# Kernel optimization log

Measured on AMD Instinct MI355X. Metric: run time of the kernel, lower is better.

Reference implementation:

```python
import jax, jax.numpy as jnp
import numpy as np

N = 50000
IN_DIM = 512
HIDDEN = 64
OUT_DIM = 47
E1 = 800000
E2 = 1200000


def setup_inputs() -> dict:
    key = jax.random.key(0)
    ks = jax.random.split(key, 10)
    x = jax.random.normal(ks[0], (N, IN_DIM), dtype=jnp.float32)
    src1 = jax.random.randint(ks[1], (E1,), 0, N, dtype=jnp.int32)
    dst1 = jax.random.randint(ks[2], (E1,), 0, N, dtype=jnp.int32)
    w1 = jax.random.uniform(ks[3], (E1,), dtype=jnp.float32)
    src2 = jax.random.randint(ks[4], (E2,), 0, N, dtype=jnp.int32)
    dst2 = jax.random.randint(ks[5], (E2,), 0, N, dtype=jnp.int32)
    w2 = jax.random.uniform(ks[6], (E2,), dtype=jnp.float32)
    embed_w = jax.random.normal(ks[7], (IN_DIM, HIDDEN), dtype=jnp.float32) / np.sqrt(IN_DIM)
    embed_b = jnp.zeros((HIDDEN,), dtype=jnp.float32)
    total_dim = (2 ** 3 - 1) * HIDDEN  # k=2 -> 7*hidden
    cls_w = jax.random.normal(ks[8], (total_dim, OUT_DIM), dtype=jnp.float32) / np.sqrt(total_dim)
    cls_b = jnp.zeros((OUT_DIM,), dtype=jnp.float32)
    return {"x": x, "src1": src1, "dst1": dst1, "w1": w1,
            "src2": src2, "dst2": dst2, "w2": w2,
            "embed_w": embed_w, "embed_b": embed_b,
            "cls_w": cls_w, "cls_b": cls_b}


def _spmm(src, dst, w, h, n):
    # out[i] = sum_{e: dst[e]==i} w[e] * h[src[e]]  == sparse_adj @ h
    return jax.ops.segment_sum(w[:, None] * h[src], dst, num_segments=n)


def reference(x, src1, dst1, w1, src2, dst2, w2, embed_w, embed_b, cls_w, cls_b):
    k = 2
    # dropout is identity in eval mode
    h = jax.nn.relu(x @ embed_w + embed_b)  # [N, hidden]
    reps = [h]
    for _ in range(k):
        h1 = _spmm(src1, dst1, w1, h, N)  # strict 1-hop
        h2 = _spmm(src2, dst2, w2, h, N)  # strict 2-hop
        h = jax.nn.relu(jnp.concatenate([h1, h2], axis=1))
        reps.append(h)
    h_final = jnp.concatenate(reps, axis=1)  # [N, 7*hidden]
    return h_final @ cls_w + cls_b
```

## Files before the change

kernel.cpp:

```cpp
#include <hip/hip_runtime.h>

#define N_NODES 50000
#define IN_DIM 512
#define HIDDEN 64
#define OUT_DIM 47
#define HSTRIDE 448

#define NBINS 391
#define CAP1 3072
#define CAP2 4096
#define CHUNK 4096

typedef unsigned short u16;
typedef short v8s __attribute__((ext_vector_type(8)));
typedef float v4f __attribute__((ext_vector_type(4)));

union F4 { float4 v; float f[4]; };
union U4 { uint4 v; unsigned u[4]; };

static __device__ __forceinline__ u16 f2bf(float f) {
  unsigned u = __float_as_uint(f);
  u += 0x7fffu + ((u >> 16) & 1u);
  return (u16)(u >> 16);
}
static __device__ __forceinline__ float bf2f(u16 h) {
  return __uint_as_float(((unsigned)h) << 16);
}

__global__ __launch_bounds__(256) void conv_w(
    const float* __restrict__ embed_w, u16* __restrict__ weTh,
    u16* __restrict__ weTl, const float* __restrict__ cls_w,
    u16* __restrict__ wcTh, u16* __restrict__ wcTl) {
  int b = blockIdx.x;
  if (b < 16) {
    int tid = b * 256 + threadIdx.x;
    int col = tid >> 6;
    int k8 = (tid & 63) * 8;
#pragma unroll
    for (int j = 0; j < 8; j++) {
      float v = embed_w[(size_t)(k8 + j) * HIDDEN + col];
      u16 h = f2bf(v);
      weTh[(size_t)col * IN_DIM + k8 + j] = h;
      weTl[(size_t)col * IN_DIM + k8 + j] = f2bf(v - bf2f(h));
    }
  } else {
    int tid = (b - 16) * 256 + threadIdx.x;
    if (tid < 48 * 56) {
      int col = tid / 56;
      int k8 = (tid % 56) * 8;
#pragma unroll
      for (int j = 0; j < 8; j++) {
        float v = (col < OUT_DIM) ? cls_w[(size_t)(k8 + j) * OUT_DIM + col] : 0.f;
        u16 h = f2bf(v);
        wcTh[(size_t)col * HSTRIDE + k8 + j] = h;
        wcTl[(size_t)col * HSTRIDE + k8 + j] = f2bf(v - bf2f(h));
      }
    }
  }
}

__global__ __launch_bounds__(256) void embed_bin(
    const float* __restrict__ x, const u16* __restrict__ wTh,
    const u16* __restrict__ wTl, const float* __restrict__ bias,
    u16* __restrict__ hcat,
    const int* __restrict__ src1, const int* __restrict__ dst1,
    const float* __restrict__ w1, int E1, int c1,
    const int* __restrict__ src2, const int* __restrict__ dst2,
    const float* __restrict__ w2, int E2,
    int* __restrict__ binCursor, int2* __restrict__ stg1,
    int2* __restrict__ stg2) {
  int b = blockIdx.x;
  if (b < 782) {
    int wave = threadIdx.x >> 6, lane = threadIdx.x & 63;
    int row0 = b * 64 + wave * 16;
    int m = lane & 15, kq = lane >> 4;
    int rowA = row0 + m;
    if (rowA >= N_NODES) rowA = N_NODES - 1;
    const float* xr = x + (size_t)rowA * IN_DIM;

    v4f acc[4];
#pragma unroll
    for (int nf = 0; nf < 4; nf++) acc[nf] = (v4f){0.f, 0.f, 0.f, 0.f};

#pragma unroll 4
    for (int k0 = 0; k0 < IN_DIM; k0 += 32) {
      int kk = k0 + kq * 8;
      F4 p, qv;
      p.v = *(const float4*)(xr + kk);
      qv.v = *(const float4*)(xr + kk + 4);
      v8s a;
#pragma unroll
      for (int j = 0; j < 4; j++) {
        a[j] = (short)f2bf(p.f[j]);
        a[4 + j] = (short)f2bf(qv.f[j]);
      }
#pragma unroll
      for (int nf = 0; nf < 4; nf++) {
        int col = nf * 16 + m;
        v8s bh = *(const v8s*)(wTh + (size_t)col * IN_DIM + kk);
        v8s bl = *(const v8s*)(wTl + (size_t)col * IN_DIM + kk);
        acc[nf] = __builtin_amdgcn_mfma_f32_16x16x32_bf16(a, bh, acc[nf], 0, 0, 0);
        acc[nf] = __builtin_amdgcn_mfma_f32_16x16x32_bf16(a, bl, acc[nf], 0, 0, 0);
      }
    }

#pragma unroll
    for (int nf = 0; nf < 4; nf++) {
      int col = nf * 16 + m;
      float bv = bias[col];
#pragma unroll
      for (int reg = 0; reg < 4; reg++) {
        int rowC = row0 + kq * 4 + reg;
        if (rowC < N_NODES) {
          float v = acc[nf][reg] + bv;
          hcat[(size_t)rowC * HSTRIDE + col] = f2bf(v > 0.f ? v : 0.f);
        }
      }
    }
    return;
  }

  int q = b - 782;
  const int *src, *dst;
  const float* w;
  int E, cap;
  int2* stg;
  int* bc;
  if (q < c1) {
    src = src1; dst = dst1; w = w1; E = E1; stg = stg1; bc = binCursor; cap = CAP1;
  } else {
    q -= c1;
    src = src2; dst = dst2; w = w2; E = E2; stg = stg2; bc = binCursor + NBINS; cap = CAP2;
  }
  int e0 = q * CHUNK;
  int n = E - e0;
  if (n > CHUNK) n = CHUNK;

  __shared__ int hist[NBINS], segrel[NBINS], cur[NBINS];
  for (int i = threadIdx.x; i < NBINS; i += 256) { hist[i] = 0; cur[i] = 0; }
  __syncthreads();
  for (int t = threadIdx.x; t < n; t += 256)
    atomicAdd(&hist[dst[e0 + t] >> 7], 1);
  __syncthreads();
  for (int i = threadIdx.x; i < NBINS; i += 256) {
    int h = hist[i];
    segrel[i] = h ? atomicAdd(&bc[i], h) : 0;
  }
  __syncthreads();
  for (int t = threadIdx.x; t < n; t += 256) {
    int d = dst[e0 + t];
    int bin = d >> 7;
    int rel = segrel[bin] + atomicAdd(&cur[bin], 1);
    if (rel < cap)
      stg[(size_t)bin * cap + rel] =
          make_int2(src[e0 + t] | ((d & 127) << 16), __float_as_int(w[e0 + t]));
  }
}

__global__ __launch_bounds__(512) void binscan(const int* __restrict__ cnt,
                                               int* __restrict__ scanout) {
  const int* in = cnt + blockIdx.x * NBINS;
  int* out = scanout + blockIdx.x * NBINS;
  int tid = threadIdx.x, lane = tid & 63, wid = tid >> 6;
  __shared__ int wsum[8];
  int v0 = (tid < NBINS) ? in[tid] : 0;
  int v = v0;
#pragma unroll
  for (int off = 1; off < 64; off <<= 1) {
    int t = __shfl_up(v, off, 64);
    if (lane >= off) v += t;
  }
  if (lane == 63) wsum[wid] = v;
  __syncthreads();
  if (tid < 8) {
    int s = wsum[tid], sc = s;
#pragma unroll
    for (int off = 1; off < 8; off <<= 1) {
      int t = __shfl_up(sc, off, 8);
      if (tid >= off) sc += t;
    }
    wsum[tid] = sc - s;
  }
  __syncthreads();
  if (tid < NBINS) out[tid] = v - v0 + wsum[wid];
}

__global__ __launch_bounds__(256) void place(
    const int* __restrict__ binCursor, const int* __restrict__ binScan,
    const int2* __restrict__ stg1, int2* __restrict__ ew1,
    int* __restrict__ ep1, const int2* __restrict__ stg2,
    int2* __restrict__ ew2, int* __restrict__ ep2) {
  int pb = blockIdx.x;
  int lb = pb < NBINS ? pb : pb - NBINS;
  const int2* stg;
  int2* ew;
  int* ep;
  int cap;
  if (pb < NBINS) { stg = stg1; ew = ew1; ep = ep1; cap = CAP1; }
  else            { stg = stg2; ew = ew2; ep = ep2; cap = CAP2; }
  int cnt = binCursor[pb];
  if (cnt > cap) cnt = cap;
  int base = binScan[pb];
  const int2* seg = stg + (size_t)lb * cap;
  int node0 = lb << 7;
  int nnodes = N_NODES - node0;
  if (nnodes > 128) nnodes = 128;

  __shared__ int ncnt[128], noff[128], ncur[128];
  __shared__ int t0;
  if (threadIdx.x < 128) { ncnt[threadIdx.x] = 0; ncur[threadIdx.x] = 0; }
  __syncthreads();
  for (int t = threadIdx.x; t < cnt; t += 256)
    atomicAdd(&ncnt[(seg[t].x >> 16) & 127], 1);
  __syncthreads();
  int v0 = 0, v = 0;
  if (threadIdx.x < 128) {
    v0 = ncnt[threadIdx.x];
    v = v0;
    int lane = threadIdx.x & 63;
#pragma unroll
    for (int off = 1; off < 64; off <<= 1) {
      int t = __shfl_up(v, off, 64);
      if (lane >= off) v += t;
    }
    if (threadIdx.x == 63) t0 = v;
  }
  __syncthreads();
  if (threadIdx.x < 128) {
    int excl = v - v0 + (threadIdx.x >= 64 ? t0 : 0);
    noff[threadIdx.x] = excl;
    if (threadIdx.x < nnodes) ep[node0 + threadIdx.x] = base + excl + v0;
  }
  __syncthreads();
  for (int t = threadIdx.x; t < cnt; t += 256) {
    int2 pk = seg[t];
    int nl = (pk.x >> 16) & 127;
    int pos = base + noff[nl] + atomicAdd(&ncur[nl], 1);
    ew[pos] = make_int2(pk.x & 0xFFFF, pk.y);
  }
}

__device__ __forceinline__ void bf8_fma(const U4& r, float wt, float* a) {
#pragma unroll
  for (int i = 0; i < 4; i++) {
    a[2 * i]     += wt * __uint_as_float(r.u[i] << 16);
    a[2 * i + 1] += wt * __uint_as_float(r.u[i] & 0xffff0000u);
  }
}

template <int NT>
__global__ __launch_bounds__(256) void gather2(
    const int* __restrict__ ep1, const int2* __restrict__ ew1,
    const int* __restrict__ ep2, const int2* __restrict__ ew2,
    const u16* __restrict__ hin, u16* __restrict__ out1,
    u16* __restrict__ out2, int half_blocks) {
  int b = blockIdx.x;
  const int* ep;
  const int2* ew;
  u16* out;
  if (b < half_blocks) { ep = ep1; ew = ew1; out = out1; }
  else { b -= half_blocks; ep = ep2; ew = ew2; out = out2; }

  int tid = b * 256 + threadIdx.x;
  int node = tid / NT;
  if (node >= N_NODES) return;
  int col0 = (tid % NT) * 8;
  int s = node ? ep[node - 1] : 0;
  int e = ep[node];

  float a0[8], a1[8];
#pragma unroll
  for (int i = 0; i < 8; i++) { a0[i] = 0.f; a1[i] = 0.f; }

  int j = s;
  for (; j + 4 <= e; j += 4) {
    int2 p0 = ew[j], p1 = ew[j + 1], p2 = ew[j + 2], p3 = ew[j + 3];
    U4 r0, r1, r2, r3;
    r0.v = *(const uint4*)(hin + (size_t)p0.x * HSTRIDE + col0);
    r1.v = *(const uint4*)(hin + (size_t)p1.x * HSTRIDE + col0);
    r2.v = *(const uint4*)(hin + (size_t)p2.x * HSTRIDE + col0);
    r3.v = *(const uint4*)(hin + (size_t)p3.x * HSTRIDE + col0);
    bf8_fma(r0, __int_as_float(p0.y), a0);
    bf8_fma(r1, __int_as_float(p1.y), a1);
    bf8_fma(r2, __int_as_float(p2.y), a0);
    bf8_fma(r3, __int_as_float(p3.y), a1);
  }
  for (; j < e; j++) {
    int2 p = ew[j];
    U4 r;
    r.v = *(const uint4*)(hin + (size_t)p.x * HSTRIDE + col0);
    bf8_fma(r, __int_as_float(p.y), a0);
  }

  U4 o;
#pragma unroll
  for (int i = 0; i < 4; i++) {
    float lo = a0[2 * i] + a1[2 * i];
    float hi = a0[2 * i + 1] + a1[2 * i + 1];
    lo = lo > 0.f ? lo : 0.f;
    hi = hi > 0.f ? hi : 0.f;
    o.u[i] = ((unsigned)f2bf(hi) << 16) | (unsigned)f2bf(lo);
  }
  *(uint4*)(out + (size_t)node * HSTRIDE + col0) = o.v;
}

__global__ __launch_bounds__(256) void final_mfma(
    const u16* __restrict__ hcat, const u16* __restrict__ wTh,
    const u16* __restrict__ wTl, const float* __restrict__ bias,
    float* __restrict__ out) {
  int wave = threadIdx.x >> 6, lane = threadIdx.x & 63;
  int row0 = blockIdx.x * 64 + wave * 16;
  int m = lane & 15, kq = lane >> 4;
  int rowA = row0 + m;
  if (rowA >= N_NODES) rowA = N_NODES - 1;
  const u16* hr = hcat + (size_t)rowA * HSTRIDE;

  v4f acc[3];
#pragma unroll
  for (int nf = 0; nf < 3; nf++) acc[nf] = (v4f){0.f, 0.f, 0.f, 0.f};

#pragma unroll 2
  for (int k0 = 0; k0 < HSTRIDE; k0 += 32) {
    int kk = k0 + kq * 8;
    v8s a = *(const v8s*)(hr + kk);
#pragma unroll
    for (int nf = 0; nf < 3; nf++) {
      int col = nf * 16 + m;
      v8s bh = *(const v8s*)(wTh + (size_t)col * HSTRIDE + kk);
      v8s bl = *(const v8s*)(wTl + (size_t)col * HSTRIDE + kk);
      acc[nf] = __builtin_amdgcn_mfma_f32_16x16x32_bf16(a, bh, acc[nf], 0, 0, 0);
      acc[nf] = __builtin_amdgcn_mfma_f32_16x16x32_bf16(a, bl, acc[nf], 0, 0, 0);
    }
  }

#pragma unroll
  for (int nf = 0; nf < 3; nf++) {
    int col = nf * 16 + m;
    if (col < OUT_DIM) {
      float bv = bias[col];
#pragma unroll
      for (int reg = 0; reg < 4; reg++) {
        int rowC = row0 + kq * 4 + reg;
        if (rowC < N_NODES)
          out[(size_t)rowC * OUT_DIM + col] = acc[nf][reg] + bv;
      }
    }
  }
}

extern "C" void kernel_launch(void* const* d_in, const int* in_sizes, int n_in,
                              void* d_out, int out_size, void* d_ws,
                              size_t ws_size, hipStream_t stream) {
  const float* x       = (const float*)d_in[0];
  const int*   src1    = (const int*)d_in[1];
  const int*   dst1    = (const int*)d_in[2];
  const float* w1      = (const float*)d_in[3];
  const int*   src2    = (const int*)d_in[4];
  const int*   dst2    = (const int*)d_in[5];
  const float* w2      = (const float*)d_in[6];
  const float* embed_w = (const float*)d_in[7];
  const float* embed_b = (const float*)d_in[8];
  const float* cls_w   = (const float*)d_in[9];
  const float* cls_b   = (const float*)d_in[10];
  int E1 = in_sizes[1];
  int E2 = in_sizes[4];

  float* ws = (float*)d_ws;
  size_t off = 0;
  u16* hcat = (u16*)(ws + off); off += (size_t)N_NODES * HSTRIDE / 2;
  int2* ew1 = (int2*)(ws + off); off += (size_t)2 * E1;
  int2* ew2 = (int2*)(ws + off); off += (size_t)2 * E2;
  int* ep1 = (int*)(ws + off); off += N_NODES;
  int* ep2 = (int*)(ws + off); off += N_NODES;
  int2* stg1 = (int2*)(ws + off); off += (size_t)2 * NBINS * CAP1;
  int2* stg2 = (int2*)(ws + off); off += (size_t)2 * NBINS * CAP2;
  int* binCursor = (int*)(ws + off); off += 2 * NBINS;
  int* binScan = (int*)(ws + off); off += 2 * NBINS;
  u16* weTh = (u16*)(ws + off); off += 16384;
  u16* weTl = (u16*)(ws + off); off += 16384;
  u16* wcTh = (u16*)(ws + off); off += 10752;
  u16* wcTl = (u16*)(ws + off); off += 10752;

  int c1 = (E1 + CHUNK - 1) / CHUNK;
  int c2 = (E2 + CHUNK - 1) / CHUNK;

  hipMemsetAsync(binCursor, 0, 2 * NBINS * sizeof(int), stream);
  conv_w<<<27, 256, 0, stream>>>(embed_w, weTh, weTl, cls_w, wcTh, wcTl);
  embed_bin<<<782 + c1 + c2, 256, 0, stream>>>(
      x, weTh, weTl, embed_b, hcat,
      src1, dst1, w1, E1, c1, src2, dst2, w2, E2,
      binCursor, stg1, stg2);
  binscan<<<2, 512, 0, stream>>>(binCursor, binScan);
  place<<<2 * NBINS, 256, 0, stream>>>(binCursor, binScan,
                                       stg1, ew1, ep1, stg2, ew2, ep2);
  gather2<8><<<3126, 256, 0, stream>>>(ep1, ew1, ep2, ew2, hcat,
                                       hcat + 64, hcat + 128, 1563);
  gather2<16><<<6250, 256, 0, stream>>>(ep1, ew1, ep2, ew2, hcat + 64,
                                        hcat + 192, hcat + 320, 3125);
  final_mfma<<<782, 256, 0, stream>>>(hcat, wcTh, wcTl, cls_b, (float*)d_out);
}
```

Before: 260.7 us.

## Stage x tiles into LDS via async global_load_lds with double buffering

The embedding GEMM now reads x through direct global-to-LDS loads (global_load_lds) into a double-buffered, XOR-swizzled shared tile. Each wave fetches the next 32-column slice while running MFMAs on the current one, instead of issuing strided float4 global loads per lane. The goal is better coalescing and overlap of x traffic with MFMA work. The cost is a __syncthreads per k-step and 16 KB of LDS shared with the binning blocks, which may lower occupancy.

Result: faster. 253.4 us (-2.8%).

```diff
diff --git a/kernel.cpp b/kernel.cpp
--- a/kernel.cpp
+++ b/kernel.cpp
@@ -25,6 +25,15 @@
 }
 static __device__ __forceinline__ float bf2f(u16 h) {
   return __uint_as_float(((unsigned)h) << 16);
+}
+
+static __device__ __forceinline__ void load_lds16(const float* g, void* l) {
+  __builtin_amdgcn_global_load_lds(
+      reinterpret_cast<const __attribute__((address_space(1))) unsigned int*>(
+          reinterpret_cast<uintptr_t>(g)),
+      reinterpret_cast<__attribute__((address_space(3))) unsigned int*>(
+          reinterpret_cast<uintptr_t>(l)),
+      16, 0, 0);
 }
 
 __global__ __launch_bounds__(256) void conv_w(
@@ -69,31 +78,61 @@
     const float* __restrict__ w2, int E2,
     int* __restrict__ binCursor, int2* __restrict__ stg1,
     int2* __restrict__ stg2) {
+  __shared__ float4 xtile4[1024];
+  __shared__ int hist[NBINS], segrel[NBINS], cur[NBINS];
   int b = blockIdx.x;
   if (b < 782) {
+    float* xtile = (float*)xtile4;
     int wave = threadIdx.x >> 6, lane = threadIdx.x & 63;
-    int row0 = b * 64 + wave * 16;
+    int row0 = b * 64;
     int m = lane & 15, kq = lane >> 4;
-    int rowA = row0 + m;
-    if (rowA >= N_NODES) rowA = N_NODES - 1;
-    const float* xr = x + (size_t)rowA * IN_DIM;
+
+    int seg0 = wave * 2;
+    int sr0 = seg0 * 8 + (lane >> 3);
+    int sr1 = sr0 + 8;
+    int sc0 = (lane & 7) ^ (sr0 & 7);
+    int sc1 = (lane & 7) ^ (sr1 & 7);
+    int gr0 = row0 + sr0; if (gr0 >= N_NODES) gr0 = N_NODES - 1;
+    int gr1 = row0 + sr1; if (gr1 >= N_NODES) gr1 = N_NODES - 1;
+    const float* g0 = x + (size_t)gr0 * IN_DIM + sc0 * 4;
+    const float* g1 = x + (size_t)gr1 * IN_DIM + sc1 * 4;
 
     v4f acc[4];
 #pragma unroll
     for (int nf = 0; nf < 4; nf++) acc[nf] = (v4f){0.f, 0.f, 0.f, 0.f};
 
-#pragma unroll 4
-    for (int k0 = 0; k0 < IN_DIM; k0 += 32) {
-      int kk = k0 + kq * 8;
-      F4 p, qv;
-      p.v = *(const float4*)(xr + kk);
-      qv.v = *(const float4*)(xr + kk + 4);
+    int r = wave * 16 + m;
+    int slotA = (2 * kq) ^ (r & 7);
+    int slotB = slotA ^ 1;
+    const float* rbase0 = (const float*)xtile + r * 32;
+    const float* rbase1 = rbase0 + 2048;
+
+    load_lds16(g0, (char*)xtile + seg0 * 1024 + (lane & 7) * 0 + 0 + (size_t)0 +
+                       (sr0 - seg0 * 8) * 0);
+    __syncthreads();
+
+    load_lds16(g1, (char*)xtile + (seg0 + 1) * 1024);
+    __syncthreads();
+
+#pragma unroll 2
+    for (int t = 0; t < 16; t++) {
+      if (t < 15) {
+        int k0n = (t + 1) * 32;
+        int bufn = (t + 1) & 1;
+        load_lds16(g0 + k0n, (char*)xtile + bufn * 8192 + seg0 * 1024);
+        load_lds16(g1 + k0n, (char*)xtile + bufn * 8192 + (seg0 + 1) * 1024);
+      }
+      const float* rb = (t & 1) ? rbase1 : rbase0;
+      F4 p, q;
+      p.v = *(const float4*)(rb + slotA * 4);
+      q.v = *(const float4*)(rb + slotB * 4);
       v8s a;
 #pragma unroll
       for (int j = 0; j < 4; j++) {
         a[j] = (short)f2bf(p.f[j]);
-        a[4 + j] = (short)f2bf(qv.f[j]);
-      }
+        a[4 + j] = (short)f2bf(q.f[j]);
+      }
+      int kk = t * 32 + kq * 8;
 #pragma unroll
       for (int nf = 0; nf < 4; nf++) {
         int col = nf * 16 + m;
@@ -102,6 +141,7 @@
         acc[nf] = __builtin_amdgcn_mfma_f32_16x16x32_bf16(a, bh, acc[nf], 0, 0, 0);
         acc[nf] = __builtin_amdgcn_mfma_f32_16x16x32_bf16(a, bl, acc[nf], 0, 0, 0);
       }
+      __syncthreads();
     }
 
 #pragma unroll
@@ -110,7 +150,7 @@
       float bv = bias[col];
 #pragma unroll
       for (int reg = 0; reg < 4; reg++) {
-        int rowC = row0 + kq * 4 + reg;
+        int rowC = row0 + wave * 16 + kq * 4 + reg;
         if (rowC < N_NODES) {
           float v = acc[nf][reg] + bv;
           hcat[(size_t)rowC * HSTRIDE + col] = f2bf(v > 0.f ? v : 0.f);
@@ -136,7 +176,6 @@
   int n = E - e0;
   if (n > CHUNK) n = CHUNK;
 
-  __shared__ int hist[NBINS], segrel[NBINS], cur[NBINS];
   for (int i = threadIdx.x; i < NBINS; i += 256) { hist[i] = 0; cur[i] = 0; }
   __syncthreads();
   for (int t = threadIdx.x; t < n; t += 256)
```

## Split embed and binning kernels; locally sort edges in LDS before coalesced staging writes

Applied to the files above, without the earlier changes.

Splits the fused embed+binning kernel into two separate launches. Edge binning now uses a smaller chunk, holds packed edges in registers, runs a block-wide prefix scan over the bin histogram, and scatters edges into an LDS buffer sorted by bin. Staging writes then go out as contiguous per-bin runs rather than scattered stores. The cost is an extra kernel launch, twice as many binning blocks competing on the global bin-cursor atomics, and the loss of overlap between the embed GEMM and binning.

New measurement: 281.0 us. 1.08x slower.

```diff
diff --git a/kernel.cpp b/kernel.cpp
--- a/kernel.cpp
+++ b/kernel.cpp
@@ -9,7 +9,7 @@
 #define NBINS 391
 #define CAP1 3072
 #define CAP2 4096
-#define CHUNK 4096
+#define CHUNK 2048
 
 typedef unsigned short u16;
 typedef short v8s __attribute__((ext_vector_type(8)));
@@ -59,68 +59,18 @@
   }
 }
 
-__global__ __launch_bounds__(256) void embed_bin(
-    const float* __restrict__ x, const u16* __restrict__ wTh,
-    const u16* __restrict__ wTl, const float* __restrict__ bias,
-    u16* __restrict__ hcat,
+__global__ __launch_bounds__(256) void bin_edges(
     const int* __restrict__ src1, const int* __restrict__ dst1,
     const float* __restrict__ w1, int E1, int c1,
     const int* __restrict__ src2, const int* __restrict__ dst2,
     const float* __restrict__ w2, int E2,
     int* __restrict__ binCursor, int2* __restrict__ stg1,
     int2* __restrict__ stg2) {
-  int b = blockIdx.x;
-  if (b < 782) {
-    int wave = threadIdx.x >> 6, lane = threadIdx.x & 63;
-    int row0 = b * 64 + wave * 16;
-    int m = lane & 15, kq = lane >> 4;
-    int rowA = row0 + m;
-    if (rowA >= N_NODES) rowA = N_NODES - 1;
-    const float* xr = x + (size_t)rowA * IN_DIM;
-
-    v4f acc[4];
-#pragma unroll
-    for (int nf = 0; nf < 4; nf++) acc[nf] = (v4f){0.f, 0.f, 0.f, 0.f};
-
-#pragma unroll 4
-    for (int k0 = 0; k0 < IN_DIM; k0 += 32) {
-      int kk = k0 + kq * 8;
-      F4 p, qv;
-      p.v = *(const float4*)(xr + kk);
-      qv.v = *(const float4*)(xr + kk + 4);
-      v8s a;
-#pragma unroll
-      for (int j = 0; j < 4; j++) {
-        a[j] = (short)f2bf(p.f[j]);
-        a[4 + j] = (short)f2bf(qv.f[j]);
-      }
-#pragma unroll
-      for (int nf = 0; nf < 4; nf++) {
-        int col = nf * 16 + m;
-        v8s bh = *(const v8s*)(wTh + (size_t)col * IN_DIM + kk);
-        v8s bl = *(const v8s*)(wTl + (size_t)col * IN_DIM + kk);
-        acc[nf] = __builtin_amdgcn_mfma_f32_16x16x32_bf16(a, bh, acc[nf], 0, 0, 0);
-        acc[nf] = __builtin_amdgcn_mfma_f32_16x16x32_bf16(a, bl, acc[nf], 0, 0, 0);
-      }
-    }
-
-#pragma unroll
-    for (int nf = 0; nf < 4; nf++) {
-      int col = nf * 16 + m;
-      float bv = bias[col];
-#pragma unroll
-      for (int reg = 0; reg < 4; reg++) {
-        int rowC = row0 + kq * 4 + reg;
-        if (rowC < N_NODES) {
-          float v = acc[nf][reg] + bv;
-          hcat[(size_t)rowC * HSTRIDE + col] = f2bf(v > 0.f ? v : 0.f);
-        }
-      }
-    }
-    return;
-  }
-
-  int q = b - 782;
+  __shared__ int hist[NBINS], sbase[NBINS], cur[NBINS], segrel[NBINS];
+  __shared__ int wsum[4];
+  __shared__ int2 buf[CHUNK];
+
+  int q = blockIdx.x;
   const int *src, *dst;
   const float* w;
   int E, cap;
@@ -135,25 +85,128 @@
   int e0 = q * CHUNK;
   int n = E - e0;
   if (n > CHUNK) n = CHUNK;
-
-  __shared__ int hist[NBINS], segrel[NBINS], cur[NBINS];
-  for (int i = threadIdx.x; i < NBINS; i += 256) { hist[i] = 0; cur[i] = 0; }
-  __syncthreads();
-  for (int t = threadIdx.x; t < n; t += 256)
-    atomicAdd(&hist[dst[e0 + t] >> 7], 1);
-  __syncthreads();
-  for (int i = threadIdx.x; i < NBINS; i += 256) {
+  int t = threadIdx.x;
+
+  for (int i = t; i < NBINS; i += 256) hist[i] = 0;
+  __syncthreads();
+
+  int2 pk[8];
+#pragma unroll
+  for (int j = 0; j < 8; j++) {
+    int idx = t + j * 256;
+    if (idx < n) {
+      int d = dst[e0 + idx];
+      int bin = d >> 7;
+      pk[j] = make_int2(src[e0 + idx] | ((d & 127) << 16) | (bin << 23),
+                        __float_as_int(w[e0 + idx]));
+      atomicAdd(&hist[bin], 1);
+    } else {
+      pk[j].x = -1;
+    }
+  }
+  __syncthreads();
+
+  int a0 = 0, a1 = 0;
+  if (t < 196) {
+    a0 = hist[2 * t];
+    if (2 * t + 1 < NBINS) a1 = hist[2 * t + 1];
+  }
+  int s = a0 + a1;
+  int lane = t & 63, wid = t >> 6;
+  int ps = s;
+#pragma unroll
+  for (int off = 1; off < 64; off <<= 1) {
+    int v = __shfl_up(ps, off, 64);
+    if (lane >= off) ps += v;
+  }
+  if (lane == 63) wsum[wid] = ps;
+  __syncthreads();
+  if (t == 0) {
+    int c = 0;
+#pragma unroll
+    for (int i = 0; i < 4; i++) { int tmp = wsum[i]; wsum[i] = c; c += tmp; }
+  }
+  __syncthreads();
+  int excl = ps - s + wsum[wid];
+  if (t < 196) {
+    sbase[2 * t] = excl;
+    cur[2 * t] = excl;
+    if (2 * t + 1 < NBINS) { sbase[2 * t + 1] = excl + a0; cur[2 * t + 1] = excl + a0; }
+  }
+  __syncthreads();
+
+#pragma unroll
+  for (int j = 0; j < 8; j++) {
+    if (pk[j].x != -1) {
+      int bin = (pk[j].x >> 23) & 0x1FF;
+      int pos = atomicAdd(&cur[bin], 1);
+      buf[pos] = pk[j];
+    }
+  }
+  for (int i = t; i < NBINS; i += 256) {
     int h = hist[i];
     segrel[i] = h ? atomicAdd(&bc[i], h) : 0;
   }
   __syncthreads();
-  for (int t = threadIdx.x; t < n; t += 256) {
-    int d = dst[e0 + t];
-    int bin = d >> 7;
-    int rel = segrel[bin] + atomicAdd(&cur[bin], 1);
-    if (rel < cap)
-      stg[(size_t)bin * cap + rel] =
-          make_int2(src[e0 + t] | ((d & 127) << 16), __float_as_int(w[e0 + t]));
+
+  for (int i = t; i < n; i += 256) {
+    int2 e = buf[i];
+    int bin = (e.x >> 23) & 0x1FF;
+    int pos = segrel[bin] + (i - sbase[bin]);
+    if (pos < cap)
+      stg[(size_t)bin * cap + pos] = make_int2(e.x & 0x7FFFFF, e.y);
+  }
+}
+
+__global__ __launch_bounds__(256) void embed_mfma(
+    const float* __restrict__ x, const u16* __restrict__ wTh,
+    const u16* __restrict__ wTl, const float* __restrict__ bias,
+    u16* __restrict__ hcat) {
+  int wave = threadIdx.x >> 6, lane = threadIdx.x & 63;
+  int row0 = blockIdx.x * 64 + wave * 16;
+  int m = lane & 15, kq = lane >> 4;
+  int rowA = row0 + m;
+  if (rowA >= N_NODES) rowA = N_NODES - 1;
+  const float* xr = x + (size_t)rowA * IN_DIM;
+
+  v4f acc[4];
+#pragma unroll
+  for (int nf = 0; nf < 4; nf++) acc[nf] = (v4f){0.f, 0.f, 0.f, 0.f};
+
+#pragma unroll 4
+  for (int k0 = 0; k0 < IN_DIM; k0 += 32) {
+    int kk = k0 + kq * 8;
+    F4 p, qv;
+    p.v = *(const float4*)(xr + kk);
+    qv.v = *(const float4*)(xr + kk + 4);
+    v8s a;
+#pragma unroll
+    for (int j = 0; j < 4; j++) {
+      a[j] = (short)f2bf(p.f[j]);
+      a[4 + j] = (short)f2bf(qv.f[j]);
+    }
+#pragma unroll
+    for (int nf = 0; nf < 4; nf++) {
+      int col = nf * 16 + m;
+      v8s bh = *(const v8s*)(wTh + (size_t)col * IN_DIM + kk);
+      v8s bl = *(const v8s*)(wTl + (size_t)col * IN_DIM + kk);
+      acc[nf] = __builtin_amdgcn_mfma_f32_16x16x32_bf16(a, bh, acc[nf], 0, 0, 0);
+      acc[nf] = __builtin_amdgcn_mfma_f32_16x16x32_bf16(a, bl, acc[nf], 0, 0, 0);
+    }
+  }
+
+#pragma unroll
+  for (int nf = 0; nf < 4; nf++) {
+    int col = nf * 16 + m;
+    float bv = bias[col];
+#pragma unroll
+    for (int reg = 0; reg < 4; reg++) {
+      int rowC = row0 + kq * 4 + reg;
+      if (rowC < N_NODES) {
+        float v = acc[nf][reg] + bv;
+        hcat[(size_t)rowC * HSTRIDE + col] = f2bf(v > 0.f ? v : 0.f);
+      }
+    }
   }
 }
 
@@ -386,10 +439,9 @@
 
   hipMemsetAsync(binCursor, 0, 2 * NBINS * sizeof(int), stream);
   conv_w<<<27, 256, 0, stream>>>(embed_w, weTh, weTl, cls_w, wcTh, wcTl);
-  embed_bin<<<782 + c1 + c2, 256, 0, stream>>>(
-      x, weTh, weTl, embed_b, hcat,
-      src1, dst1, w1, E1, c1, src2, dst2, w2, E2,
-      binCursor, stg1, stg2);
+  bin_edges<<<c1 + c2, 256, 0, stream>>>(
+      src1, dst1, w1, E1, c1, src2, dst2, w2, E2, binCursor, stg1, stg2);
+  embed_mfma<<<782, 256, 0, stream>>>(x, weTh, weTl, embed_b, hcat);
   binscan<<<2, 512, 0, stream>>>(binCursor, binScan);
   place<<<2 * NBINS, 256, 0, stream>>>(binCursor, binScan,
                                        stg1, ew1, ep1, stg2, ew2, ep2);
```
